# Optimization experiments

Hardware: AMD Instinct MI355X
Metric: run time of the kernel (lower is better)

The kernel has to match this reference:

```python
import jax, jax.numpy as jnp
import numpy as np

GROUPS = 16
GROUP_SIZE = 16
K = 3
KK = K * K
BN_EPS = 1e-5


def setup_inputs() -> dict:
    key = jax.random.key(0)
    ks = jax.random.split(key, 6)
    B, C, H, W = 16, 256, 56, 56
    mid = C // 4  # rd_ratio = 4
    x = jax.random.normal(ks[0], (B, C, H, W), dtype=jnp.float32)
    w1 = jax.random.normal(ks[1], (mid, C), dtype=jnp.float32) * (1.0 / np.sqrt(C))
    bn_gamma = jnp.ones((mid,), dtype=jnp.float32)
    bn_beta = jnp.zeros((mid,), dtype=jnp.float32)
    bn_mean = jax.random.normal(ks[2], (mid,), dtype=jnp.float32) * 0.1
    bn_var = jax.random.uniform(ks[3], (mid,), dtype=jnp.float32, minval=0.5, maxval=1.5)
    w2 = jax.random.normal(ks[4], (KK * GROUPS, mid), dtype=jnp.float32) * (1.0 / np.sqrt(mid))
    b2 = jax.random.normal(ks[5], (KK * GROUPS,), dtype=jnp.float32) * 0.01
    return {"x": x, "w1": w1, "bn_gamma": bn_gamma, "bn_beta": bn_beta,
            "bn_mean": bn_mean, "bn_var": bn_var, "w2": w2, "b2": b2}


def reference(x, w1, bn_gamma, bn_beta, bn_mean, bn_var, w2, b2):
    B, C, H, W = x.shape
    # conv1: 1x1 conv + BatchNorm (eval) + ReLU
    t = jnp.einsum('bchw,oc->bohw', x, w1)
    scale = bn_gamma / jnp.sqrt(bn_var + BN_EPS)
    t = t * scale[None, :, None, None] + (bn_beta - bn_mean * scale)[None, :, None, None]
    t = jax.nn.relu(t)
    # conv2: 1x1 conv producing per-pixel kernels (B, KK*groups, H, W)
    weight = jnp.einsum('bchw,oc->bohw', t, w2) + b2[None, :, None, None]
    weight = weight.reshape(B, GROUPS, 1, KK, H, W)
    # unfold: extract 3x3 patches (pad=1, stride=1), kernel positions row-major
    xp = jnp.pad(x, ((0, 0), (0, 0), (1, 1), (1, 1)))
    patches = jnp.stack(
        [xp[:, :, i:i + H, j:j + W] for i in range(K) for j in range(K)],
        axis=2)  # (B, C, KK, H, W), matches torch unfold's (c*KK + kk) layout
    patches = patches.reshape(B, GROUPS, GROUP_SIZE, KK, H, W)
    out = (weight * patches).sum(axis=3).reshape(B, C, H, W)
    return out
```

## Files before the change

### kernel.cpp

```cpp
#include <hip/hip_runtime.h>


#define Cn    256
#define MID   64
#define Hn    56
#define Wn    56
#define HW    3136
#define Bn    16
#define NPIX  (Bn * HW)
#define CHW   (Cn * HW)
#define NKK   9
#define NG    16
#define GSZ   16
#define PXT   64
#define BN_EPS 1e-5f

#define GLOAD_LDS(src, dst, sz)                                                        \
  __builtin_amdgcn_global_load_lds(                                                    \
      (const __attribute__((address_space(1))) void*)(src),                            \
      (__attribute__((address_space(3))) void*)(dst), (sz), 0, 0)

__global__ __launch_bounds__(256) void prep_kernel(
    const float* __restrict__ w1,
    const float* __restrict__ gamma,
    const float* __restrict__ beta,
    const float* __restrict__ mean,
    const float* __restrict__ var,
    float* __restrict__ w1f,
    float* __restrict__ bias1) {
  int idx = blockIdx.x * 256 + threadIdx.x;
  if (idx < MID * Cn) {
    int c = idx >> 6;
    int o = idx & 63;
    float scale = gamma[o] / sqrtf(var[o] + BN_EPS);
    w1f[idx] = w1[o * Cn + c] * scale;
  } else if (idx < MID * Cn + MID) {
    int o = idx - MID * Cn;
    float scale = gamma[o] / sqrtf(var[o] + BN_EPS);
    bias1[o] = beta[o] - mean[o] * scale;
  }
}

__global__ __launch_bounds__(256) void conv1_kernel(
    const float* __restrict__ x,
    const float* __restrict__ w1f,
    const float* __restrict__ bias1,
    float* __restrict__ t) {
  __shared__ __align__(16) float lx[3][16][PXT];

  const int tid = threadIdx.x;
  const int px  = tid & 63;
  const int wv  = __builtin_amdgcn_readfirstlane(tid >> 6);

  const int bid = blockIdx.x;
  const int px0 = bid * PXT;
  const int b   = px0 / HW;
  const int hw0 = px0 - b * HW;
  const float* xb = x + (size_t)b * CHW + hw0;

  const int rsub = px >> 4;
  const int csub = (px & 15) << 2;
  const int lrow = (wv << 2) + rsub;

  GLOAD_LDS(xb + (size_t)lrow * HW + csub, &lx[0][wv << 2][0], 16);
  GLOAD_LDS(xb + (size_t)(16 + lrow) * HW + csub, &lx[1][wv << 2][0], 16);

  float acc[16];
#pragma unroll
  for (int j = 0; j < 16; ++j) acc[j] = 0.0f;

  for (int k = 0; k < 16; ++k) {
    if (k < 15) {
      asm volatile("s_waitcnt vmcnt(1)" ::: "memory");
    } else {
      asm volatile("s_waitcnt vmcnt(0)" ::: "memory");
    }
    __builtin_amdgcn_s_barrier();
    __builtin_amdgcn_sched_barrier(0);
    if (k < 14) {
      const int nb = (k + 2) % 3;
      GLOAD_LDS(xb + (size_t)((k + 2) * 16 + lrow) * HW + csub,
                &lx[nb][wv << 2][0], 16);
    }
    const float* lxk = &lx[k % 3][0][0];
    const float* wr0 = w1f + (k << 10) + (wv << 4);
#pragma unroll
    for (int c = 0; c < 16; ++c) {
      const float xv = lxk[(c << 6) + px];
      const float* wr = wr0 + (c << 6);
      const float4 wa = *(const float4*)(wr + 0);
      const float4 wb = *(const float4*)(wr + 4);
      const float4 wc = *(const float4*)(wr + 8);
      const float4 wd = *(const float4*)(wr + 12);
      acc[0]  = fmaf(xv, wa.x, acc[0]);
      acc[1]  = fmaf(xv, wa.y, acc[1]);
      acc[2]  = fmaf(xv, wa.z, acc[2]);
      acc[3]  = fmaf(xv, wa.w, acc[3]);
      acc[4]  = fmaf(xv, wb.x, acc[4]);
      acc[5]  = fmaf(xv, wb.y, acc[5]);
      acc[6]  = fmaf(xv, wb.z, acc[6]);
      acc[7]  = fmaf(xv, wb.w, acc[7]);
      acc[8]  = fmaf(xv, wc.x, acc[8]);
      acc[9]  = fmaf(xv, wc.y, acc[9]);
      acc[10] = fmaf(xv, wc.z, acc[10]);
      acc[11] = fmaf(xv, wc.w, acc[11]);
      acc[12] = fmaf(xv, wd.x, acc[12]);
      acc[13] = fmaf(xv, wd.y, acc[13]);
      acc[14] = fmaf(xv, wd.z, acc[14]);
      acc[15] = fmaf(xv, wd.w, acc[15]);
    }
  }

#pragma unroll
  for (int j = 0; j < 16; ++j) {
    const int o = (wv << 4) + j;
    t[(size_t)o * NPIX + px0 + px] = fmaxf(acc[j] + bias1[o], 0.0f);
  }
}

#define LOADCH(dst, ch)                                                   \
  {                                                                       \
    const float* _xp = xcg + (size_t)(ch) * HW;                           \
    _Pragma("unroll")                                                     \
    for (int kk = 0; kk < NKK; ++kk) dst[kk] = _xp[off[kk]];              \
  }
#define CONSUME(src, ch)                                                  \
  {                                                                       \
    float s0 = wk[0] * src[0];                                            \
    float s1 = wk[1] * src[1];                                            \
    float s2 = wk[2] * src[2];                                            \
    s0 = fmaf(wk[3], src[3], s0);                                         \
    s1 = fmaf(wk[4], src[4], s1);                                         \
    s2 = fmaf(wk[5], src[5], s2);                                         \
    s0 = fmaf(wk[6], src[6], s0);                                         \
    s1 = fmaf(wk[7], src[7], s1);                                         \
    s2 = fmaf(wk[8], src[8], s2);                                         \
    res[ch] = s0 + s1 + s2;                                               \
  }

__global__ __launch_bounds__(256, 4) void conv2_inv_kernel(
    const float* __restrict__ x,
    const float* __restrict__ t,
    const float* __restrict__ w2,
    const float* __restrict__ b2,
    float* __restrict__ out) {
  __shared__ __align__(16) float lt[MID][PXT];

  const int tid = threadIdx.x;
  const int px  = tid & 63;
  const int wv  = __builtin_amdgcn_readfirstlane(tid >> 6);

  const int bid = blockIdx.x;
  const int pc  = ((bid >> 5) << 3) + (bid & 7);
  const int gq  = (bid >> 3) & 3;
  const int g   = (gq << 2) + wv;

  const int px0 = pc * PXT;
  const int b   = px0 / HW;
  const int hw0 = px0 - b * HW;

  const int rsub = px >> 4;
  const int csub = (px & 15) << 2;

#pragma unroll
  for (int j = 0; j < 4; ++j) {
    const int r0 = (wv << 4) + (j << 2);
    GLOAD_LDS(t + (size_t)(r0 + rsub) * NPIX + px0 + csub, &lt[r0][0], 16);
  }

  const int hw = hw0 + px;
  const int h  = hw / Wn;
  const int w  = hw - h * Wn;

  int off[NKK];
  unsigned vmask = 0;
#pragma unroll
  for (int kk = 0; kk < NKK; ++kk) {
    const int di  = kk / 3 - 1;
    const int dj  = kk % 3 - 1;
    const int h2  = h + di;
    const int w2v = w + dj;
    const bool valid = ((unsigned)h2 < (unsigned)Hn) && ((unsigned)w2v < (unsigned)Wn);
    off[kk] = valid ? (h2 * Wn + w2v) : hw;
    vmask |= (valid ? 1u : 0u) << kk;
  }

  const float* xcg = x + (size_t)b * CHW + (size_t)(g * GSZ) * HW;
  float p0[NKK], p1[NKK], p2[NKK], p3[NKK];
  LOADCH(p0, 0)
  LOADCH(p1, 1)
  LOADCH(p2, 2)
  LOADCH(p3, 3)

  __syncthreads();

  float a[NKK];
#pragma unroll
  for (int kk = 0; kk < NKK; ++kk) a[kk] = b2[g * NKK + kk];

  const float* wg = w2 + (size_t)g * (NKK * MID);
#pragma unroll 4
  for (int o4 = 0; o4 < MID; o4 += 4) {
    const float t0 = lt[o4 + 0][px];
    const float t1 = lt[o4 + 1][px];
    const float t2 = lt[o4 + 2][px];
    const float t3 = lt[o4 + 3][px];
#pragma unroll
    for (int kk = 0; kk < NKK; ++kk) {
      const float4 w4 = *(const float4*)(wg + (kk << 6) + o4);
      a[kk] = fmaf(t3, w4.w, fmaf(t2, w4.z, fmaf(t1, w4.y, fmaf(t0, w4.x, a[kk]))));
    }
  }

  float wk[NKK];
#pragma unroll
  for (int kk = 0; kk < NKK; ++kk)
    wk[kk] = ((vmask >> kk) & 1u) ? a[kk] : 0.0f;

  float res[GSZ];

  CONSUME(p0, 0)  LOADCH(p0, 4)
  CONSUME(p1, 1)  LOADCH(p1, 5)
  CONSUME(p2, 2)  LOADCH(p2, 6)
  CONSUME(p3, 3)  LOADCH(p3, 7)
  CONSUME(p0, 4)  LOADCH(p0, 8)
  CONSUME(p1, 5)  LOADCH(p1, 9)
  CONSUME(p2, 6)  LOADCH(p2, 10)
  CONSUME(p3, 7)  LOADCH(p3, 11)
  CONSUME(p0, 8)  LOADCH(p0, 12)
  CONSUME(p1, 9)  LOADCH(p1, 13)
  CONSUME(p2, 10) LOADCH(p2, 14)
  CONSUME(p3, 11) LOADCH(p3, 15)
  CONSUME(p0, 12)
  CONSUME(p1, 13)
  CONSUME(p2, 14)
  CONSUME(p3, 15)

  float* ob = out + (size_t)b * CHW + (size_t)(g * GSZ) * HW + hw;
#pragma unroll
  for (int cc = 0; cc < GSZ; ++cc)
    ob[(size_t)cc * HW] = res[cc];
}

extern "C" void kernel_launch(void* const* d_in, const int* in_sizes, int n_in,
                              void* d_out, int out_size, void* d_ws, size_t ws_size,
                              hipStream_t stream) {
  const float* x     = (const float*)d_in[0];
  const float* w1    = (const float*)d_in[1];
  const float* gamma = (const float*)d_in[2];
  const float* beta  = (const float*)d_in[3];
  const float* mean  = (const float*)d_in[4];
  const float* var   = (const float*)d_in[5];
  const float* w2    = (const float*)d_in[6];
  const float* b2    = (const float*)d_in[7];
  float* out = (float*)d_out;

  char* ws = (char*)d_ws;
  float* t     = (float*)ws;
  float* w1f   = (float*)(ws + (size_t)MID * NPIX * 4);
  float* bias1 = (float*)(ws + (size_t)MID * NPIX * 4 + (size_t)MID * Cn * 4);

  prep_kernel<<<(MID * Cn + MID + 255) / 256, 256, 0, stream>>>(
      w1, gamma, beta, mean, var, w1f, bias1);
  conv1_kernel<<<NPIX / PXT, 256, 0, stream>>>(x, w1f, bias1, t);
  conv2_inv_kernel<<<NPIX / PXT * 4, 256, 0, stream>>>(x, t, w2, b2, out);
}
```

Measured before the change: 159.3 us.

## Use single-wave blocks per group in conv2, loading t directly into registers

New measurement: 179.3 us. 1.13x slower.

```diff
diff --git a/kernel.cpp b/kernel.cpp
--- a/kernel.cpp
+++ b/kernel.cpp
@@ -120,9 +120,9 @@
 
 #define LOADCH(dst, ch)                                                   \
   {                                                                       \
-    const float* _xp = xcg + (size_t)(ch) * HW;                           \
     _Pragma("unroll")                                                     \
-    for (int kk = 0; kk < NKK; ++kk) dst[kk] = _xp[off[kk]];              \
+    for (int kk = 0; kk < NKK; ++kk)                                      \
+      dst[kk] = xg[(unsigned)((ch) * HW) + off[kk]];                      \
   }
 #define CONSUME(src, ch)                                                  \
   {                                                                       \
@@ -135,44 +135,38 @@
     s0 = fmaf(wk[6], src[6], s0);                                         \
     s1 = fmaf(wk[7], src[7], s1);                                         \
     s2 = fmaf(wk[8], src[8], s2);                                         \
-    res[ch] = s0 + s1 + s2;                                               \
-  }
-
-__global__ __launch_bounds__(256, 4) void conv2_inv_kernel(
+    og[(unsigned)((ch) * HW) + hw] = s0 + s1 + s2;                        \
+  }
+
+__global__ __launch_bounds__(64, 4) void conv2_inv_kernel(
     const float* __restrict__ x,
     const float* __restrict__ t,
     const float* __restrict__ w2,
     const float* __restrict__ b2,
     float* __restrict__ out) {
-  __shared__ __align__(16) float lt[MID][PXT];
-
-  const int tid = threadIdx.x;
-  const int px  = tid & 63;
-  const int wv  = __builtin_amdgcn_readfirstlane(tid >> 6);
+  const unsigned px = threadIdx.x;
 
   const int bid = blockIdx.x;
-  const int pc  = ((bid >> 5) << 3) + (bid & 7);
-  const int gq  = (bid >> 3) & 3;
-  const int g   = (gq << 2) + wv;
-
-  const int px0 = pc * PXT;
-  const int b   = px0 / HW;
-  const int hw0 = px0 - b * HW;
-
-  const int rsub = px >> 4;
-  const int csub = (px & 15) << 2;
-
-#pragma unroll
-  for (int j = 0; j < 4; ++j) {
-    const int r0 = (wv << 4) + (j << 2);
-    GLOAD_LDS(t + (size_t)(r0 + rsub) * NPIX + px0 + csub, &lt[r0][0], 16);
-  }
-
-  const int hw = hw0 + px;
-  const int h  = hw / Wn;
-  const int w  = hw - h * Wn;
-
-  int off[NKK];
+  const int r   = bid & 7;
+  const int kq  = bid >> 3;
+  const int g   = kq & 15;
+  const int pc  = ((kq >> 4) << 3) + r;
+
+  const int b   = pc / 49;
+  const unsigned hw = (unsigned)(pc - b * 49) * PXT + px;
+
+  const float* __restrict__ tb = t + (size_t)pc * PXT;
+
+  float tv[32], tw[32];
+#pragma unroll
+  for (int o = 0; o < 32; ++o) tv[o] = tb[(unsigned)(o * NPIX) + px];
+#pragma unroll
+  for (int o = 0; o < 32; ++o) tw[o] = tb[(unsigned)((o + 32) * NPIX) + px];
+
+  const int h = hw / Wn;
+  const int w = hw - h * Wn;
+
+  unsigned off[NKK];
   unsigned vmask = 0;
 #pragma unroll
   for (int kk = 0; kk < NKK; ++kk) {
@@ -181,34 +175,45 @@
     const int h2  = h + di;
     const int w2v = w + dj;
     const bool valid = ((unsigned)h2 < (unsigned)Hn) && ((unsigned)w2v < (unsigned)Wn);
-    off[kk] = valid ? (h2 * Wn + w2v) : hw;
+    off[kk] = valid ? (unsigned)(h2 * Wn + w2v) : hw;
     vmask |= (valid ? 1u : 0u) << kk;
   }
 
-  const float* xcg = x + (size_t)b * CHW + (size_t)(g * GSZ) * HW;
+  float a[NKK];
+#pragma unroll
+  for (int kk = 0; kk < NKK; ++kk) a[kk] = b2[g * NKK + kk];
+
+  const float* wg = w2 + (size_t)g * (NKK * MID);
+
+#pragma unroll
+  for (int o4 = 0; o4 < 32; o4 += 4) {
+#pragma unroll
+    for (int kk = 0; kk < NKK; ++kk) {
+      const float4 w4 = *(const float4*)(wg + (kk << 6) + o4);
+      a[kk] = fmaf(tv[o4 + 3], w4.w,
+              fmaf(tv[o4 + 2], w4.z,
+              fmaf(tv[o4 + 1], w4.y,
+              fmaf(tv[o4 + 0], w4.x, a[kk]))));
+    }
+  }
+
+  const float* __restrict__ xg = x + (size_t)b * CHW + (size_t)(g * GSZ) * HW;
+  float* __restrict__ og = out + (size_t)b * CHW + (size_t)(g * GSZ) * HW;
   float p0[NKK], p1[NKK], p2[NKK], p3[NKK];
   LOADCH(p0, 0)
   LOADCH(p1, 1)
   LOADCH(p2, 2)
   LOADCH(p3, 3)
 
-  __syncthreads();
-
-  float a[NKK];
-#pragma unroll
-  for (int kk = 0; kk < NKK; ++kk) a[kk] = b2[g * NKK + kk];
-
-  const float* wg = w2 + (size_t)g * (NKK * MID);
-#pragma unroll 4
-  for (int o4 = 0; o4 < MID; o4 += 4) {
-    const float t0 = lt[o4 + 0][px];
-    const float t1 = lt[o4 + 1][px];
-    const float t2 = lt[o4 + 2][px];
-    const float t3 = lt[o4 + 3][px];
+#pragma unroll
+  for (int o4 = 0; o4 < 32; o4 += 4) {
 #pragma unroll
     for (int kk = 0; kk < NKK; ++kk) {
-      const float4 w4 = *(const float4*)(wg + (kk << 6) + o4);
-      a[kk] = fmaf(t3, w4.w, fmaf(t2, w4.z, fmaf(t1, w4.y, fmaf(t0, w4.x, a[kk]))));
+      const float4 w4 = *(const float4*)(wg + (kk << 6) + 32 + o4);
+      a[kk] = fmaf(tw[o4 + 3], w4.w,
+              fmaf(tw[o4 + 2], w4.z,
+              fmaf(tw[o4 + 1], w4.y,
+              fmaf(tw[o4 + 0], w4.x, a[kk]))));
     }
   }
 
@@ -216,8 +221,6 @@
 #pragma unroll
   for (int kk = 0; kk < NKK; ++kk)
     wk[kk] = ((vmask >> kk) & 1u) ? a[kk] : 0.0f;
-
-  float res[GSZ];
 
   CONSUME(p0, 0)  LOADCH(p0, 4)
   CONSUME(p1, 1)  LOADCH(p1, 5)
@@ -235,11 +238,6 @@
   CONSUME(p1, 13)
   CONSUME(p2, 14)
   CONSUME(p3, 15)
-
-  float* ob = out + (size_t)b * CHW + (size_t)(g * GSZ) * HW + hw;
-#pragma unroll
-  for (int cc = 0; cc < GSZ; ++cc)
-    ob[(size_t)cc * HW] = res[cc];
 }
 
 extern "C" void kernel_launch(void* const* d_in, const int* in_sizes, int n_in,
@@ -263,5 +261,5 @@
   prep_kernel<<<(MID * Cn + MID + 255) / 256, 256, 0, stream>>>(
       w1, gamma, beta, mean, var, w1f, bias1);
   conv1_kernel<<<NPIX / PXT, 256, 0, stream>>>(x, w1f, bias1, t);
-  conv2_inv_kernel<<<NPIX / PXT * 4, 256, 0, stream>>>(x, t, w2, b2, out);
-}
+  conv2_inv_kernel<<<NPIX / PXT * NG, 64, 0, stream>>>(x, t, w2, b2, out);
+}
```

## Store intermediate t pixel-major and read it directly as float4 in conv2

Applied to the files above, without the earlier changes.

Result: slower. 177.0 us (+11.1%).

```diff
diff --git a/kernel.cpp b/kernel.cpp
--- a/kernel.cpp
+++ b/kernel.cpp
@@ -111,10 +111,14 @@
     }
   }
 
-#pragma unroll
-  for (int j = 0; j < 16; ++j) {
-    const int o = (wv << 4) + j;
-    t[(size_t)o * NPIX + px0 + px] = fmaxf(acc[j] + bias1[o], 0.0f);
+  float4* tp = (float4*)(t + ((size_t)(px0 + px) << 6) + (wv << 4));
+#pragma unroll
+  for (int q = 0; q < 4; ++q) {
+    const int o = (wv << 4) + (q << 2);
+    tp[q] = make_float4(fmaxf(acc[q * 4 + 0] + bias1[o + 0], 0.0f),
+                        fmaxf(acc[q * 4 + 1] + bias1[o + 1], 0.0f),
+                        fmaxf(acc[q * 4 + 2] + bias1[o + 2], 0.0f),
+                        fmaxf(acc[q * 4 + 3] + bias1[o + 3], 0.0f));
   }
 }
 
@@ -137,6 +141,31 @@
     s2 = fmaf(wk[8], src[8], s2);                                         \
     res[ch] = s0 + s1 + s2;                                               \
   }
+#define C2CHUNK(Q)                                                        \
+  {                                                                       \
+    const float4 ta = tc[(Q) * 4 + 0];                                    \
+    const float4 tb_ = tc[(Q) * 4 + 1];                                   \
+    const float4 tcc = tc[(Q) * 4 + 2];                                   \
+    const float4 td = tc[(Q) * 4 + 3];                                    \
+    _Pragma("unroll")                                                     \
+    for (int kk = 0; kk < NKK; ++kk) {                                    \
+      const float* _w = wg + (kk << 6) + (Q) * 16;                        \
+      const float4 wA = *(const float4*)(_w + 0);                         \
+      const float4 wB = *(const float4*)(_w + 4);                         \
+      const float4 wC = *(const float4*)(_w + 8);                         \
+      const float4 wD = *(const float4*)(_w + 12);                        \
+      float s = fmaf(ta.x, wA.x, a[kk]);                                  \
+      s = fmaf(ta.y, wA.y, s);  s = fmaf(ta.z, wA.z, s);                  \
+      s = fmaf(ta.w, wA.w, s);  s = fmaf(tb_.x, wB.x, s);                 \
+      s = fmaf(tb_.y, wB.y, s); s = fmaf(tb_.z, wB.z, s);                 \
+      s = fmaf(tb_.w, wB.w, s); s = fmaf(tcc.x, wC.x, s);                 \
+      s = fmaf(tcc.y, wC.y, s); s = fmaf(tcc.z, wC.z, s);                 \
+      s = fmaf(tcc.w, wC.w, s); s = fmaf(td.x, wD.x, s);                  \
+      s = fmaf(td.y, wD.y, s);  s = fmaf(td.z, wD.z, s);                  \
+      s = fmaf(td.w, wD.w, s);                                            \
+      a[kk] = s;                                                          \
+    }                                                                     \
+  }
 
 __global__ __launch_bounds__(256, 4) void conv2_inv_kernel(
     const float* __restrict__ x,
@@ -144,8 +173,6 @@
     const float* __restrict__ w2,
     const float* __restrict__ b2,
     float* __restrict__ out) {
-  __shared__ __align__(16) float lt[MID][PXT];
-
   const int tid = threadIdx.x;
   const int px  = tid & 63;
   const int wv  = __builtin_amdgcn_readfirstlane(tid >> 6);
@@ -159,14 +186,7 @@
   const int b   = px0 / HW;
   const int hw0 = px0 - b * HW;
 
-  const int rsub = px >> 4;
-  const int csub = (px & 15) << 2;
-
-#pragma unroll
-  for (int j = 0; j < 4; ++j) {
-    const int r0 = (wv << 4) + (j << 2);
-    GLOAD_LDS(t + (size_t)(r0 + rsub) * NPIX + px0 + csub, &lt[r0][0], 16);
-  }
+  const float4* __restrict__ tc = (const float4*)(t + ((size_t)(px0 + px) << 6));
 
   const int hw = hw0 + px;
   const int h  = hw / Wn;
@@ -185,39 +205,30 @@
     vmask |= (valid ? 1u : 0u) << kk;
   }
 
+  float a[NKK];
+#pragma unroll
+  for (int kk = 0; kk < NKK; ++kk) a[kk] = b2[g * NKK + kk];
+
+  const float* wg = w2 + (size_t)g * (NKK * MID);
+
+  C2CHUNK(0)
+  C2CHUNK(1)
+  C2CHUNK(2)
+  C2CHUNK(3)
+
+  float wk[NKK];
+#pragma unroll
+  for (int kk = 0; kk < NKK; ++kk)
+    wk[kk] = ((vmask >> kk) & 1u) ? a[kk] : 0.0f;
+
   const float* xcg = x + (size_t)b * CHW + (size_t)(g * GSZ) * HW;
   float p0[NKK], p1[NKK], p2[NKK], p3[NKK];
+  float res[GSZ];
+
   LOADCH(p0, 0)
   LOADCH(p1, 1)
   LOADCH(p2, 2)
   LOADCH(p3, 3)
-
-  __syncthreads();
-
-  float a[NKK];
-#pragma unroll
-  for (int kk = 0; kk < NKK; ++kk) a[kk] = b2[g * NKK + kk];
-
-  const float* wg = w2 + (size_t)g * (NKK * MID);
-#pragma unroll 4
-  for (int o4 = 0; o4 < MID; o4 += 4) {
-    const float t0 = lt[o4 + 0][px];
-    const float t1 = lt[o4 + 1][px];
-    const float t2 = lt[o4 + 2][px];
-    const float t3 = lt[o4 + 3][px];
-#pragma unroll
-    for (int kk = 0; kk < NKK; ++kk) {
-      const float4 w4 = *(const float4*)(wg + (kk << 6) + o4);
-      a[kk] = fmaf(t3, w4.w, fmaf(t2, w4.z, fmaf(t1, w4.y, fmaf(t0, w4.x, a[kk]))));
-    }
-  }
-
-  float wk[NKK];
-#pragma unroll
-  for (int kk = 0; kk < NKK; ++kk)
-    wk[kk] = ((vmask >> kk) & 1u) ? a[kk] : 0.0f;
-
-  float res[GSZ];
 
   CONSUME(p0, 0)  LOADCH(p0, 4)
   CONSUME(p1, 1)  LOADCH(p1, 5)
```
